# Kernel optimization log

Measured on AMD Instinct MI355X. Metric: run time of the kernel, lower is better.

Reference implementation:

```python
import jax, jax.numpy as jnp
import numpy as np

T, U, I, B, K = 64, 142, 4500, 16384, 10


def setup_inputs() -> dict:
    key = jax.random.key(0)
    k1, k2, k3, k4, k5, k6 = jax.random.split(key, 6)
    q = jax.random.uniform(k1, (T, U, I), dtype=jnp.float32, minval=0.01, maxval=5.0)
    miss = jax.random.uniform(k2, (T, U, I)) < 0.3
    qos_tensor = jnp.where(miss, 0.0, q)
    # user_avg exactly as in __init__: sum over items / count of rated items (clamped >= 1)
    cnt = jnp.clip((qos_tensor > 0).sum(axis=2).astype(jnp.float32), 1.0, None)
    user_avg = qos_tensor.sum(axis=2) / cnt  # [T, U]
    # time-aggregated similarity: random symmetric matrix in [-1, 1]
    s = jax.random.uniform(k3, (U, U), dtype=jnp.float32, minval=-1.0, maxval=1.0)
    user_sim_agg = 0.5 * (s + s.T)
    user_id = jax.random.randint(k4, (B,), 0, U)
    item_id = jax.random.randint(k5, (B,), 0, I)
    time_id = jax.random.randint(k6, (B,), 0, T)
    return {
        "qos_tensor": qos_tensor,
        "user_avg": user_avg,
        "user_sim_agg": user_sim_agg,
        "user_id": user_id,
        "item_id": item_id,
        "time_id": time_id,
        "top_k": K,
    }


def reference(qos_tensor, user_avg, user_sim_agg, user_id, item_id, time_id, top_k):
    num_users = qos_tensor.shape[1]
    avg_u = user_avg[time_id, user_id]                      # [B]
    sim_u = user_sim_agg[user_id]                           # [B, U]
    # ratings of every user for (time_id, item_id): column gather, [B, U]
    u_idx = jnp.arange(num_users)[None, :]
    item_col = qos_tensor[time_id[:, None], u_idx, item_id[:, None]]
    item_rated = item_col > 0                               # [B, U]
    sim_m = jnp.where(item_rated, sim_u, 0.0)
    top_sim, top_user = jax.lax.top_k(sim_m, top_k)         # [B, K]
    top_sim = top_sim / (top_sim.sum(axis=1, keepdims=True) + 1e-8)
    top_sim = jnp.nan_to_num(top_sim)
    # neighbor ratings and neighbor averages
    r_vs = qos_tensor[time_id[:, None], top_user, item_id[:, None]]  # [B, K]
    avg_v = user_avg[time_id[:, None], top_user]                     # [B, K]
    pred = avg_u + (top_sim * (r_vs - avg_v)).sum(axis=1)            # [B]
    return pred
```

## Files before the change

### kernel.cpp

```cpp
#include <hip/hip_runtime.h>
#include <math.h>

#define T_DIM 64
#define U_DIM 142
#define I_DIM 4500
#define B_DIM 16384
#define K_TOP 10

__global__ __launch_bounds__(256) void ucf_kernel(
    const float* __restrict__ qos,
    const float* __restrict__ user_avg,
    const float* __restrict__ user_sim,
    const int*   __restrict__ user_id,
    const int*   __restrict__ item_id,
    const int*   __restrict__ time_id,
    float*       __restrict__ out)
{
    const int lane = threadIdx.x & 63;
    const int wid  = threadIdx.x >> 6;
    const int b    = blockIdx.x * 4 + wid;
    if (b >= B_DIM) return;

    const int u = user_id[b];
    const int i = item_id[b];
    const int t = time_id[b];

    const float* qcol = qos + ((size_t)t * U_DIM) * (size_t)I_DIM + i;
    const float* srow = user_sim + (size_t)u * U_DIM;
    const float* arow = user_avg + (size_t)t * U_DIM;

    float val[3];
    float con[3];
#pragma unroll
    for (int j = 0; j < 3; ++j) {
        const int v = lane + j * 64;
        float sv = -INFINITY;
        float cv = 0.0f;
        if (v < U_DIM) {
            const float rv = qcol[(size_t)v * I_DIM];
            const float av = arow[v];
            const float s  = srow[v];
            sv = (rv > 0.0f) ? s : 0.0f;
            cv = sv * (rv - av);
        }
        val[j] = sv;
        con[j] = cv;
    }

    float ssum = 0.0f;
    float wsum = 0.0f;
#pragma unroll
    for (int k = 0; k < K_TOP; ++k) {
        float mv = val[0]; float mc = con[0]; int mk = lane;
        if (val[1] > mv) { mv = val[1]; mc = con[1]; mk = lane + 64; }
        if (val[2] > mv) { mv = val[2]; mc = con[2]; mk = lane + 128; }
#pragma unroll
        for (int off = 32; off > 0; off >>= 1) {
            const float ov = __shfl_xor(mv, off, 64);
            const float oc = __shfl_xor(mc, off, 64);
            const int   ok = __shfl_xor(mk, off, 64);
            if (ov > mv || (ov == mv && ok < mk)) { mv = ov; mc = oc; mk = ok; }
        }
        ssum += mv;
        wsum += mc;
        if ((mk & 63) == lane) {
            const int slot = mk >> 6;
            if (slot == 0)      val[0] = -INFINITY;
            else if (slot == 1) val[1] = -INFINITY;
            else                val[2] = -INFINITY;
        }
    }

    if (lane == 0) {
        const float avg_u = arow[u];
        out[b] = avg_u + wsum / (ssum + 1e-8f);
    }
}

extern "C" void kernel_launch(void* const* d_in, const int* in_sizes, int n_in,
                              void* d_out, int out_size, void* d_ws, size_t ws_size,
                              hipStream_t stream) {
    const float* qos  = (const float*)d_in[0];
    const float* uavg = (const float*)d_in[1];
    const float* usim = (const float*)d_in[2];
    const int*   uid  = (const int*)d_in[3];
    const int*   iid  = (const int*)d_in[4];
    const int*   tid  = (const int*)d_in[5];
    float* out = (float*)d_out;

    dim3 block(256);
    dim3 grid(B_DIM / 4);
    ucf_kernel<<<grid, block, 0, stream>>>(qos, uavg, usim, uid, iid, tid, out);
}
```

Before: 247.1 us.

## Transpose QoS tensor into workspace so per-query user columns are contiguous

Adds a kernel that transposes the whole QoS tensor into a [T, I, padded U] layout in the workspace, so each query's 142-user column becomes one contiguous read instead of 142 strided loads. The top-k loop now shuffles only value and index and fetches the selected contribution with a single shuffle. In exchange, every call reads and writes the entire ~164MB tensor, far more traffic than the ~16K×142 scattered gathers it replaces. It falls back to the old kernel when the workspace is too small.

```diff
diff --git a/kernel.cpp b/kernel.cpp
--- a/kernel.cpp
+++ b/kernel.cpp
@@ -6,6 +6,142 @@
 #define I_DIM 4500
 #define B_DIM 16384
 #define K_TOP 10
+
+#define PADU  160
+#define NT_I  71
+#define NT_V  3
+
+__global__ __launch_bounds__(256) void transpose_kernel(
+    const float* __restrict__ qos,
+    float*       __restrict__ qt)
+{
+    __shared__ float tile[64][65];
+
+    const int blk  = blockIdx.x;
+    const int it   = blk % NT_I;
+    const int rest = blk / NT_I;
+    const int vt   = rest % NT_V;
+    const int t    = rest / NT_V;
+    const int i0   = it * 64;
+    const int v0   = vt * 64;
+
+    const int il = (threadIdx.x & 15) * 4;
+    const int vl = threadIdx.x >> 4;
+#pragma unroll
+    for (int r = 0; r < 4; ++r) {
+        const int v = v0 + vl + 16 * r;
+        const int i = i0 + il;
+        float4 d = make_float4(0.0f, 0.0f, 0.0f, 0.0f);
+        if (v < U_DIM) {
+            const float* src = qos + ((size_t)t * U_DIM + v) * I_DIM + i;
+            if (i + 3 < I_DIM) {
+                d = *(const float4*)src;
+            } else {
+                if (i + 0 < I_DIM) d.x = src[0];
+                if (i + 1 < I_DIM) d.y = src[1];
+                if (i + 2 < I_DIM) d.z = src[2];
+                if (i + 3 < I_DIM) d.w = src[3];
+            }
+        }
+        const int vr = vl + 16 * r;
+        tile[vr][il + 0] = d.x;
+        tile[vr][il + 1] = d.y;
+        tile[vr][il + 2] = d.z;
+        tile[vr][il + 3] = d.w;
+    }
+    __syncthreads();
+
+    const int wx = threadIdx.x & 63;
+    const int wy = threadIdx.x >> 6;
+    const int v  = v0 + wx;
+    if (v < U_DIM) {
+#pragma unroll
+        for (int r = 0; r < 16; ++r) {
+            const int i = i0 + wy + 4 * r;
+            if (i < I_DIM)
+                qt[((size_t)t * I_DIM + i) * PADU + v] = tile[wx][wy + 4 * r];
+        }
+    }
+}
+
+__global__ __launch_bounds__(256) void ucf_kernel_t(
+    const float* __restrict__ qt,
+    const float* __restrict__ user_avg,
+    const float* __restrict__ user_sim,
+    const int*   __restrict__ user_id,
+    const int*   __restrict__ item_id,
+    const int*   __restrict__ time_id,
+    float*       __restrict__ out)
+{
+    const int lane = threadIdx.x & 63;
+    const int wid  = threadIdx.x >> 6;
+    const int b    = blockIdx.x * 4 + wid;
+    if (b >= B_DIM) return;
+
+    const int u = user_id[b];
+    const int i = item_id[b];
+    const int t = time_id[b];
+
+    const float* qcol = qt + ((size_t)t * I_DIM + i) * PADU;
+    const float* srow = user_sim + (size_t)u * U_DIM;
+    const float* arow = user_avg + (size_t)t * U_DIM;
+
+    float val0 = -INFINITY, val1 = -INFINITY, val2 = -INFINITY;
+    float con0 = 0.0f, con1 = 0.0f, con2 = 0.0f;
+    {
+        const int v0 = lane;
+        const int v1 = lane + 64;
+        const int v2 = lane + 128;
+        const float rv0 = qcol[v0];
+        const float rv1 = qcol[v1];
+        const float a0  = arow[v0];
+        const float a1  = arow[v1];
+        const float s0  = srow[v0];
+        const float s1  = srow[v1];
+        val0 = (rv0 > 0.0f) ? s0 : 0.0f;
+        con0 = val0 * (rv0 - a0);
+        val1 = (rv1 > 0.0f) ? s1 : 0.0f;
+        con1 = val1 * (rv1 - a1);
+        if (v2 < U_DIM) {
+            const float rv2 = qcol[v2];
+            const float a2  = arow[v2];
+            const float s2  = srow[v2];
+            val2 = (rv2 > 0.0f) ? s2 : 0.0f;
+            con2 = val2 * (rv2 - a2);
+        }
+    }
+
+    float ssum = 0.0f;
+    float wsum = 0.0f;
+#pragma unroll
+    for (int k = 0; k < K_TOP; ++k) {
+        float mv = val0; int mk = lane;
+        if (val1 > mv) { mv = val1; mk = lane + 64; }
+        if (val2 > mv) { mv = val2; mk = lane + 128; }
+#pragma unroll
+        for (int off = 32; off > 0; off >>= 1) {
+            const float ov = __shfl_xor(mv, off, 64);
+            const int   ok = __shfl_xor(mk, off, 64);
+            if (ov > mv || (ov == mv && ok < mk)) { mv = ov; mk = ok; }
+        }
+        const int slot = mk >> 6;
+        const int wl   = mk & 63;
+        const float csel = (slot == 0) ? con0 : (slot == 1) ? con1 : con2;
+        const float mc = __shfl(csel, wl, 64);
+        ssum += mv;
+        wsum += mc;
+        if (wl == lane) {
+            if (slot == 0)      val0 = -INFINITY;
+            else if (slot == 1) val1 = -INFINITY;
+            else                val2 = -INFINITY;
+        }
+    }
+
+    if (lane == 0) {
+        const float avg_u = arow[u];
+        out[b] = avg_u + wsum / (ssum + 1e-8f);
+    }
+}
 
 __global__ __launch_bounds__(256) void ucf_kernel(
     const float* __restrict__ qos,
@@ -88,7 +224,15 @@
     const int*   tid  = (const int*)d_in[5];
     float* out = (float*)d_out;
 
-    dim3 block(256);
-    dim3 grid(B_DIM / 4);
-    ucf_kernel<<<grid, block, 0, stream>>>(qos, uavg, usim, uid, iid, tid, out);
-}
+    const size_t qt_bytes = (size_t)T_DIM * I_DIM * PADU * sizeof(float);
+
+    if (d_ws != nullptr && ws_size >= qt_bytes) {
+        float* qt = (float*)d_ws;
+        transpose_kernel<<<dim3(T_DIM * NT_V * NT_I), dim3(256), 0, stream>>>(qos, qt);
+        ucf_kernel_t<<<dim3(B_DIM / 4), dim3(256), 0, stream>>>(
+            qt, uavg, usim, uid, iid, tid, out);
+    } else {
+        ucf_kernel<<<dim3(B_DIM / 4), dim3(256), 0, stream>>>(
+            qos, uavg, usim, uid, iid, tid, out);
+    }
+}
```

After: 320.2 us. +29.6%, slower.

## Bucket queries by time and item chunk to stream coalesced QoS tiles

Applied to the files above, without the earlier changes.

Adds an index-building pass that groups queries by (time, 256-item chunk), then one block per cell streams the contiguous QoS tile for all users with float4 loads into LDS and answers each query from LDS. This replaces strided per-query column gathers that waste most of each cache line. Overflowed queries fall back to a cleanup kernel. It adds extra launches, atomics and workspace use, and it reads the whole tensor regardless of query density.

```diff
diff --git a/kernel.cpp b/kernel.cpp
--- a/kernel.cpp
+++ b/kernel.cpp
@@ -6,6 +6,236 @@
 #define I_DIM 4500
 #define B_DIM 16384
 #define K_TOP 10
+
+#define CHW   256
+#define NCH   18
+#define NCELL (T_DIM * NCH)
+#define CAPC  48
+#define SROW  145
+
+#define CNT_OFF   0
+#define OVFC_OFF  (NCELL)
+#define OVF_OFF   (NCELL + 1)
+#define LIST_OFF  (OVF_OFF + B_DIM)
+#define WS_INTS   (LIST_OFF + NCELL * CAPC)
+#define WS_BYTES  ((size_t)WS_INTS * sizeof(int))
+
+__global__ void zero_ws(int* __restrict__ ws)
+{
+    for (int k = threadIdx.x; k <= NCELL; k += 256) ws[CNT_OFF + k] = 0;
+}
+
+__global__ __launch_bounds__(256) void build_index(
+    const int* __restrict__ time_id,
+    const int* __restrict__ item_id,
+    int*       __restrict__ ws)
+{
+    const int b = blockIdx.x * 256 + threadIdx.x;
+    if (b >= B_DIM) return;
+    const int t = time_id[b];
+    const int c = item_id[b] >> 8;
+    const int cell = t * NCH + c;
+    const int j = atomicAdd(&ws[CNT_OFF + cell], 1);
+    if (j < CAPC) {
+        ws[LIST_OFF + cell * CAPC + j] = b;
+    } else {
+        const int k = atomicAdd(&ws[OVFC_OFF], 1);
+        ws[OVF_OFF + k] = b;
+    }
+}
+
+__global__ __launch_bounds__(256) void ucf_stream(
+    const float* __restrict__ qos,
+    const float* __restrict__ user_avg,
+    const float* __restrict__ user_sim,
+    const int*   __restrict__ user_id,
+    const int*   __restrict__ item_id,
+    int*         __restrict__ ws,
+    float*       __restrict__ out)
+{
+    __shared__ float lds[CAPC * SROW];
+    __shared__ int   ls_b[CAPC];
+    __shared__ int   ls_u[CAPC];
+    __shared__ int   ls_i[CAPC];
+
+    const int cell = blockIdx.x;
+    const int t    = cell / NCH;
+    const int c    = cell - t * NCH;
+    const int i0   = c * CHW;
+    const int W    = (I_DIM - i0 < CHW) ? (I_DIM - i0) : CHW;
+
+    int cnt = ws[CNT_OFF + cell];
+    if (cnt > CAPC) cnt = CAPC;
+    if (cnt == 0) return;
+
+    const int lane = threadIdx.x & 63;
+    const int wid  = threadIdx.x >> 6;
+
+    if (threadIdx.x < cnt) {
+        const int b = ws[LIST_OFF + cell * CAPC + threadIdx.x];
+        ls_b[threadIdx.x] = b;
+        ls_u[threadIdx.x] = user_id[b];
+        ls_i[threadIdx.x] = item_id[b];
+    }
+    __syncthreads();
+
+    unsigned int pk0 = 0, pk1 = 0;
+    int nOwn = 0;
+    for (int s = 0; s < cnt; ++s) {
+        const int di = ls_i[s] - i0;
+        if ((di >> 2) == lane) {
+            if (nOwn < 8) {
+                const unsigned e = (unsigned)((s << 2) | (di & 3));
+                if (nOwn < 4) pk0 |= e << (8 * nOwn);
+                else          pk1 |= e << (8 * (nOwn - 4));
+                ++nOwn;
+            } else if (wid == 0) {
+                const int k = atomicAdd(&ws[OVFC_OFF], 1);
+                ws[OVF_OFF + k] = ls_b[s];
+            }
+        }
+    }
+
+    const float* base = qos + ((size_t)t * U_DIM) * (size_t)I_DIM + i0 + lane * 4;
+    const bool doload = (lane * 4) < W;
+    for (int v = wid; v < U_DIM; v += 4) {
+        float4 q = make_float4(0.f, 0.f, 0.f, 0.f);
+        if (doload) q = *(const float4*)(base + (size_t)v * I_DIM);
+        for (int e = 0; e < nOwn; ++e) {
+            const unsigned pk = (e < 4) ? (pk0 >> (8 * e)) : (pk1 >> (8 * (e - 4)));
+            const int s  = (pk >> 2) & 0x3f;
+            const int el = pk & 3;
+            const float val = (el == 0) ? q.x : (el == 1) ? q.y : (el == 2) ? q.z : q.w;
+            lds[s * SROW + v] = val;
+        }
+    }
+    __syncthreads();
+
+    const float* arow = user_avg + (size_t)t * U_DIM;
+    for (int s = wid; s < cnt; s += 4) {
+        const int b = ls_b[s];
+        const int u = ls_u[s];
+        const float* srow = user_sim + (size_t)u * U_DIM;
+        const float* col  = lds + s * SROW;
+
+        float val0, val1, val2 = -INFINITY;
+        float con0, con1, con2 = 0.0f;
+        {
+            const float rv0 = col[lane];
+            const float rv1 = col[lane + 64];
+            const float a0  = arow[lane];
+            const float a1  = arow[lane + 64];
+            const float s0  = srow[lane];
+            const float s1  = srow[lane + 64];
+            val0 = (rv0 > 0.0f) ? s0 : 0.0f;
+            con0 = val0 * (rv0 - a0);
+            val1 = (rv1 > 0.0f) ? s1 : 0.0f;
+            con1 = val1 * (rv1 - a1);
+            if (lane + 128 < U_DIM) {
+                const float rv2 = col[lane + 128];
+                const float a2  = arow[lane + 128];
+                const float s2  = srow[lane + 128];
+                val2 = (rv2 > 0.0f) ? s2 : 0.0f;
+                con2 = val2 * (rv2 - a2);
+            }
+        }
+
+        float ssum = 0.0f, wsum = 0.0f;
+#pragma unroll
+        for (int k = 0; k < K_TOP; ++k) {
+            float mv = val0; int mk = lane;
+            if (val1 > mv) { mv = val1; mk = lane + 64; }
+            if (val2 > mv) { mv = val2; mk = lane + 128; }
+#pragma unroll
+            for (int off = 32; off > 0; off >>= 1) {
+                const float ov = __shfl_xor(mv, off, 64);
+                const int   ok = __shfl_xor(mk, off, 64);
+                if (ov > mv || (ov == mv && ok < mk)) { mv = ov; mk = ok; }
+            }
+            const int sl = mk >> 6;
+            const int wl = mk & 63;
+            const float csel = (sl == 0) ? con0 : (sl == 1) ? con1 : con2;
+            const float mc = __shfl(csel, wl, 64);
+            ssum += mv;
+            wsum += mc;
+            if (wl == lane) {
+                if (sl == 0)      val0 = -INFINITY;
+                else if (sl == 1) val1 = -INFINITY;
+                else              val2 = -INFINITY;
+            }
+        }
+
+        if (lane == 0) out[b] = arow[u] + wsum / (ssum + 1e-8f);
+    }
+}
+
+__global__ __launch_bounds__(256) void ucf_cleanup(
+    const float* __restrict__ qos,
+    const float* __restrict__ user_avg,
+    const float* __restrict__ user_sim,
+    const int*   __restrict__ user_id,
+    const int*   __restrict__ item_id,
+    const int*   __restrict__ time_id,
+    const int*   __restrict__ ws,
+    float*       __restrict__ out)
+{
+    const int lane = threadIdx.x & 63;
+    const int wid  = threadIdx.x >> 6;
+    const int nw   = gridDim.x * 4;
+    const int w0   = blockIdx.x * 4 + wid;
+    const int ovfc = ws[OVFC_OFF];
+
+    for (int k = w0; k < ovfc; k += nw) {
+        const int b = ws[OVF_OFF + k];
+        const int u = user_id[b];
+        const int i = item_id[b];
+        const int t = time_id[b];
+        const float* qcol = qos + ((size_t)t * U_DIM) * (size_t)I_DIM + i;
+        const float* srow = user_sim + (size_t)u * U_DIM;
+        const float* arow = user_avg + (size_t)t * U_DIM;
+
+        float val0, val1, val2 = -INFINITY;
+        float con0, con1, con2 = 0.0f;
+        {
+            const float rv0 = qcol[(size_t)lane * I_DIM];
+            const float rv1 = qcol[(size_t)(lane + 64) * I_DIM];
+            val0 = (rv0 > 0.0f) ? srow[lane] : 0.0f;
+            con0 = val0 * (rv0 - arow[lane]);
+            val1 = (rv1 > 0.0f) ? srow[lane + 64] : 0.0f;
+            con1 = val1 * (rv1 - arow[lane + 64]);
+            if (lane + 128 < U_DIM) {
+                const float rv2 = qcol[(size_t)(lane + 128) * I_DIM];
+                val2 = (rv2 > 0.0f) ? srow[lane + 128] : 0.0f;
+                con2 = val2 * (rv2 - arow[lane + 128]);
+            }
+        }
+        float ssum = 0.0f, wsum = 0.0f;
+#pragma unroll
+        for (int kk = 0; kk < K_TOP; ++kk) {
+            float mv = val0; int mk = lane;
+            if (val1 > mv) { mv = val1; mk = lane + 64; }
+            if (val2 > mv) { mv = val2; mk = lane + 128; }
+#pragma unroll
+            for (int off = 32; off > 0; off >>= 1) {
+                const float ov = __shfl_xor(mv, off, 64);
+                const int   ok = __shfl_xor(mk, off, 64);
+                if (ov > mv || (ov == mv && ok < mk)) { mv = ov; mk = ok; }
+            }
+            const int sl = mk >> 6;
+            const int wl = mk & 63;
+            const float csel = (sl == 0) ? con0 : (sl == 1) ? con1 : con2;
+            const float mc = __shfl(csel, wl, 64);
+            ssum += mv;
+            wsum += mc;
+            if (wl == lane) {
+                if (sl == 0)      val0 = -INFINITY;
+                else if (sl == 1) val1 = -INFINITY;
+                else              val2 = -INFINITY;
+            }
+        }
+        if (lane == 0) out[b] = arow[u] + wsum / (ssum + 1e-8f);
+    }
+}
 
 __global__ __launch_bounds__(256) void ucf_kernel(
     const float* __restrict__ qos,
@@ -47,8 +277,7 @@
         con[j] = cv;
     }
 
-    float ssum = 0.0f;
-    float wsum = 0.0f;
+    float ssum = 0.0f, wsum = 0.0f;
 #pragma unroll
     for (int k = 0; k < K_TOP; ++k) {
         float mv = val[0]; float mc = con[0]; int mk = lane;
@@ -72,8 +301,7 @@
     }
 
     if (lane == 0) {
-        const float avg_u = arow[u];
-        out[b] = avg_u + wsum / (ssum + 1e-8f);
+        out[b] = arow[u] + wsum / (ssum + 1e-8f);
     }
 }
 
@@ -88,7 +316,16 @@
     const int*   tid  = (const int*)d_in[5];
     float* out = (float*)d_out;
 
-    dim3 block(256);
-    dim3 grid(B_DIM / 4);
-    ucf_kernel<<<grid, block, 0, stream>>>(qos, uavg, usim, uid, iid, tid, out);
-}
+    if (d_ws != nullptr && ws_size >= WS_BYTES) {
+        int* ws = (int*)d_ws;
+        zero_ws<<<dim3(1), dim3(256), 0, stream>>>(ws);
+        build_index<<<dim3((B_DIM + 255) / 256), dim3(256), 0, stream>>>(tid, iid, ws);
+        ucf_stream<<<dim3(NCELL), dim3(256), 0, stream>>>(
+            qos, uavg, usim, uid, iid, ws, out);
+        ucf_cleanup<<<dim3(16), dim3(256), 0, stream>>>(
+            qos, uavg, usim, uid, iid, tid, ws, out);
+    } else {
+        ucf_kernel<<<dim3(B_DIM / 4), dim3(256), 0, stream>>>(
+            qos, uavg, usim, uid, iid, tid, out);
+    }
+}
```

Result: slower. 297.7 us (+20.5%).

## Process two queries per wavefront and shuffle contribution only for the winner

Applied to the files above, without the earlier changes.

Each wavefront now handles two batch entries and issues all six strided qos gathers for both before computing, so more memory loads are in flight per wave. The top-k reduction no longer shuffles the contribution value at every butterfly step; it fetches it once per selected element with an indexed shuffle. In exchange, register pressure rises and there are half as many waves.

```diff
diff --git a/kernel.cpp b/kernel.cpp
--- a/kernel.cpp
+++ b/kernel.cpp
@@ -7,7 +7,7 @@
 #define B_DIM 16384
 #define K_TOP 10
 
-__global__ __launch_bounds__(256) void ucf_kernel(
+__global__ __launch_bounds__(256) void ucf2_kernel(
     const float* __restrict__ qos,
     const float* __restrict__ user_avg,
     const float* __restrict__ user_sim,
@@ -18,62 +18,123 @@
 {
     const int lane = threadIdx.x & 63;
     const int wid  = threadIdx.x >> 6;
-    const int b    = blockIdx.x * 4 + wid;
-    if (b >= B_DIM) return;
+    const int w    = blockIdx.x * 4 + wid;
+    const int b0   = w;
+    const int b1   = w + (B_DIM / 2);
 
-    const int u = user_id[b];
-    const int i = item_id[b];
-    const int t = time_id[b];
+    const int u0 = user_id[b0], u1 = user_id[b1];
+    const int i0 = item_id[b0], i1 = item_id[b1];
+    const int t0 = time_id[b0], t1 = time_id[b1];
 
-    const float* qcol = qos + ((size_t)t * U_DIM) * (size_t)I_DIM + i;
-    const float* srow = user_sim + (size_t)u * U_DIM;
-    const float* arow = user_avg + (size_t)t * U_DIM;
+    const float* qcol0 = qos + ((size_t)t0 * U_DIM) * (size_t)I_DIM + i0;
+    const float* qcol1 = qos + ((size_t)t1 * U_DIM) * (size_t)I_DIM + i1;
 
-    float val[3];
-    float con[3];
-#pragma unroll
-    for (int j = 0; j < 3; ++j) {
-        const int v = lane + j * 64;
-        float sv = -INFINITY;
-        float cv = 0.0f;
-        if (v < U_DIM) {
-            const float rv = qcol[(size_t)v * I_DIM];
-            const float av = arow[v];
-            const float s  = srow[v];
-            sv = (rv > 0.0f) ? s : 0.0f;
-            cv = sv * (rv - av);
-        }
-        val[j] = sv;
-        con[j] = cv;
+    const float rA0 = qcol0[(size_t)lane * I_DIM];
+    const float rA1 = qcol0[(size_t)(lane + 64) * I_DIM];
+    const float rB0 = qcol1[(size_t)lane * I_DIM];
+    const float rB1 = qcol1[(size_t)(lane + 64) * I_DIM];
+    float rA2 = 0.0f, rB2 = 0.0f;
+    const bool has2 = (lane + 128) < U_DIM;
+    if (has2) {
+        rA2 = qcol0[(size_t)(lane + 128) * I_DIM];
+        rB2 = qcol1[(size_t)(lane + 128) * I_DIM];
     }
 
-    float ssum = 0.0f;
-    float wsum = 0.0f;
+    const float* arow0 = user_avg + (size_t)t0 * U_DIM;
+    const float* arow1 = user_avg + (size_t)t1 * U_DIM;
+    const float* srow0 = user_sim + (size_t)u0 * U_DIM;
+    const float* srow1 = user_sim + (size_t)u1 * U_DIM;
+
+    {
+        float val0, val1, val2 = -INFINITY;
+        float con0, con1, con2 = 0.0f;
+        {
+            const float a0 = arow0[lane];
+            const float a1 = arow0[lane + 64];
+            const float s0 = srow0[lane];
+            const float s1 = srow0[lane + 64];
+            val0 = (rA0 > 0.0f) ? s0 : 0.0f;
+            con0 = val0 * (rA0 - a0);
+            val1 = (rA1 > 0.0f) ? s1 : 0.0f;
+            con1 = val1 * (rA1 - a1);
+            if (has2) {
+                const float a2 = arow0[lane + 128];
+                const float s2 = srow0[lane + 128];
+                val2 = (rA2 > 0.0f) ? s2 : 0.0f;
+                con2 = val2 * (rA2 - a2);
+            }
+        }
+        float ssum = 0.0f, wsum = 0.0f;
 #pragma unroll
-    for (int k = 0; k < K_TOP; ++k) {
-        float mv = val[0]; float mc = con[0]; int mk = lane;
-        if (val[1] > mv) { mv = val[1]; mc = con[1]; mk = lane + 64; }
-        if (val[2] > mv) { mv = val[2]; mc = con[2]; mk = lane + 128; }
+        for (int k = 0; k < K_TOP; ++k) {
+            float mv = val0; int mk = lane;
+            if (val1 > mv) { mv = val1; mk = lane + 64; }
+            if (val2 > mv) { mv = val2; mk = lane + 128; }
 #pragma unroll
-        for (int off = 32; off > 0; off >>= 1) {
-            const float ov = __shfl_xor(mv, off, 64);
-            const float oc = __shfl_xor(mc, off, 64);
-            const int   ok = __shfl_xor(mk, off, 64);
-            if (ov > mv || (ov == mv && ok < mk)) { mv = ov; mc = oc; mk = ok; }
+            for (int off = 32; off > 0; off >>= 1) {
+                const float ov = __shfl_xor(mv, off, 64);
+                const int   ok = __shfl_xor(mk, off, 64);
+                if (ov > mv || (ov == mv && ok < mk)) { mv = ov; mk = ok; }
+            }
+            const int sl = mk >> 6;
+            const int wl = mk & 63;
+            const float csel = (sl == 0) ? con0 : (sl == 1) ? con1 : con2;
+            const float mc = __shfl(csel, wl, 64);
+            ssum += mv;
+            wsum += mc;
+            if (wl == lane) {
+                if (sl == 0)      val0 = -INFINITY;
+                else if (sl == 1) val1 = -INFINITY;
+                else              val2 = -INFINITY;
+            }
         }
-        ssum += mv;
-        wsum += mc;
-        if ((mk & 63) == lane) {
-            const int slot = mk >> 6;
-            if (slot == 0)      val[0] = -INFINITY;
-            else if (slot == 1) val[1] = -INFINITY;
-            else                val[2] = -INFINITY;
-        }
+        if (lane == 0) out[b0] = arow0[u0] + wsum / (ssum + 1e-8f);
     }
 
-    if (lane == 0) {
-        const float avg_u = arow[u];
-        out[b] = avg_u + wsum / (ssum + 1e-8f);
+    {
+        float val0, val1, val2 = -INFINITY;
+        float con0, con1, con2 = 0.0f;
+        {
+            const float a0 = arow1[lane];
+            const float a1 = arow1[lane + 64];
+            const float s0 = srow1[lane];
+            const float s1 = srow1[lane + 64];
+            val0 = (rB0 > 0.0f) ? s0 : 0.0f;
+            con0 = val0 * (rB0 - a0);
+            val1 = (rB1 > 0.0f) ? s1 : 0.0f;
+            con1 = val1 * (rB1 - a1);
+            if (has2) {
+                const float a2 = arow1[lane + 128];
+                const float s2 = srow1[lane + 128];
+                val2 = (rB2 > 0.0f) ? s2 : 0.0f;
+                con2 = val2 * (rB2 - a2);
+            }
+        }
+        float ssum = 0.0f, wsum = 0.0f;
+#pragma unroll
+        for (int k = 0; k < K_TOP; ++k) {
+            float mv = val0; int mk = lane;
+            if (val1 > mv) { mv = val1; mk = lane + 64; }
+            if (val2 > mv) { mv = val2; mk = lane + 128; }
+#pragma unroll
+            for (int off = 32; off > 0; off >>= 1) {
+                const float ov = __shfl_xor(mv, off, 64);
+                const int   ok = __shfl_xor(mk, off, 64);
+                if (ov > mv || (ov == mv && ok < mk)) { mv = ov; mk = ok; }
+            }
+            const int sl = mk >> 6;
+            const int wl = mk & 63;
+            const float csel = (sl == 0) ? con0 : (sl == 1) ? con1 : con2;
+            const float mc = __shfl(csel, wl, 64);
+            ssum += mv;
+            wsum += mc;
+            if (wl == lane) {
+                if (sl == 0)      val0 = -INFINITY;
+                else if (sl == 1) val1 = -INFINITY;
+                else              val2 = -INFINITY;
+            }
+        }
+        if (lane == 0) out[b1] = arow1[u1] + wsum / (ssum + 1e-8f);
     }
 }
 
@@ -89,6 +150,6 @@
     float* out = (float*)d_out;
 
     dim3 block(256);
-    dim3 grid(B_DIM / 4);
-    ucf_kernel<<<grid, block, 0, stream>>>(qos, uavg, usim, uid, iid, tid, out);
+    dim3 grid(B_DIM / 8);
+    ucf2_kernel<<<grid, block, 0, stream>>>(qos, uavg, usim, uid, iid, tid, out);
 }
```

New measurement: 251.8 us. No clear change (+1.9%).
